# Optimization experiments

Measured on AMD Instinct MI355X. Metric: run time of the kernel, lower is better.

## Reference

```python
import jax, jax.numpy as jnp
import numpy as np

E, C_IN, NUM_CLASSES = 4, 3, 100
HW = 32
C1, C2, GC = 64, 128, 16
FC_IN = C2 * (HW // 4) * (HW // 4)  # 128*8*8 = 8192


def _conv(x, w, b):
    # x: [B,Cin,H,W], w: [Cout,Cin,3,3] -> [B,Cout,H,W] (SAME padding)
    y = jax.lax.conv_general_dilated(x, w, (1, 1), 'SAME',
                                     dimension_numbers=('NCHW', 'OIHW', 'NCHW'))
    return y + b[None, :, None, None]


def _maxpool2(x):
    return jax.lax.reduce_window(x, -jnp.inf, jax.lax.max,
                                 (1, 1, 2, 2), (1, 1, 2, 2), 'VALID')


def setup_inputs() -> dict:
    key = jax.random.key(0)
    ks = jax.random.split(key, 12)
    s = lambda k, shape, fan: (jax.random.normal(k, shape, jnp.float32) / np.sqrt(fan))
    return {
        'x': jax.random.normal(ks[0], (1024, C_IN, HW, HW), jnp.float32),
        # gating network
        'gate_cw': s(ks[1], (GC, C_IN, 3, 3), C_IN * 9),
        'gate_cb': jnp.zeros((GC,), jnp.float32),
        'gate_fw': s(ks[2], (E, GC), GC),
        'gate_fb': jnp.zeros((E,), jnp.float32),
        # stacked expert params [E, ...]
        'e_c1w': s(ks[3], (E, C1, C_IN, 3, 3), C_IN * 9),
        'e_c1b': jnp.zeros((E, C1), jnp.float32),
        'e_c2w': s(ks[4], (E, C2, C1, 3, 3), C1 * 9),
        'e_c2b': jnp.zeros((E, C2), jnp.float32),
        'e_fw': s(ks[5], (E, NUM_CLASSES, FC_IN), FC_IN),
        'e_fb': jnp.zeros((E, NUM_CLASSES), jnp.float32),
    }


def reference(x, gate_cw, gate_cb, gate_fw, gate_fb,
              e_c1w, e_c1b, e_c2w, e_c2b, e_fw, e_fb):
    B = x.shape[0]
    # --- gating: conv -> relu -> global avg pool -> linear -> softmax ---
    g = jax.nn.relu(_conv(x, gate_cw, gate_cb))            # [B,GC,H,W]
    g = g.mean(axis=(2, 3))                                # [B,GC]
    router_probs = jax.nn.softmax(g @ gate_fw.T + gate_fb) # [B,E]

    best_weights = router_probs.max(axis=1)                # [B]
    best_indices = jnp.argmax(router_probs, axis=1)        # [B]

    # --- hard top-1 dispatch: mask-and-combine (same math as gather/scatter) ---
    final_output = jnp.zeros((B, NUM_CLASSES), x.dtype)
    for e in range(E):  # fixed small expert count, structurally distinct params
        h = jax.nn.relu(_conv(x, e_c1w[e], e_c1b[e]))      # [B,64,32,32]
        h = _maxpool2(h)                                   # [B,64,16,16]
        h = jax.nn.relu(_conv(h, e_c2w[e], e_c2b[e]))      # [B,128,16,16]
        h = _maxpool2(h)                                   # [B,128,8,8]
        logits = h.reshape(B, -1) @ e_fw[e].T + e_fb[e]    # [B,100]
        mask = (best_indices == e)[:, None]
        final_output = final_output + jnp.where(
            mask, logits * best_weights[:, None], 0.0)

    mean_probs = router_probs.mean(axis=0)
    aux_loss = jnp.mean((mean_probs - 1.0 / E) ** 2)
    return final_output, router_probs, aux_loss
```

## Files before the change

### kernel.cpp

```cpp
#include <hip/hip_runtime.h>
#include <hip/hip_bf16.h>
#include <cstdint>


#define B_TOT 1024

typedef __attribute__((ext_vector_type(8))) short short8;
typedef __attribute__((ext_vector_type(16))) float f32x16;

__device__ __forceinline__ ushort f2bf(float f) {
  uint32_t u = __float_as_uint(f);
  u += 0x7fffu + ((u >> 16) & 1u);
  return (ushort)(u >> 16);
}

__global__ __launch_bounds__(256) void k_prep(
    const float* __restrict__ x, const float* __restrict__ gcw,
    const float* __restrict__ gcb, const float* __restrict__ gfw,
    const float* __restrict__ gfb, float* __restrict__ probs,
    float* __restrict__ best_w, int* __restrict__ best_idx,
    const float* __restrict__ w2, ushort* __restrict__ wp,
    const float* __restrict__ w1, ushort* __restrict__ wA,
    const float* __restrict__ efw, ushort* __restrict__ wfc) {
  __shared__ float xs[3 * 34 * 34];
  __shared__ float red[4 * 16];
  __shared__ float gm[16];
  __shared__ float lgs[4];
  const int blk = blockIdx.x;
  const int t = threadIdx.x;

  if (blk < 1024) {
    const int b = blk;
    const float* xb = x + (size_t)b * 3072;

    for (int c = t; c < 3468; c += 256) {
      const int ci = c / 1156;
      const int rem = c - ci * 1156;
      const int y = rem / 34;
      const int xx = rem - y * 34;
      const int gy = y - 1, gx = xx - 1;
      float v = 0.f;
      if (gy >= 0 && gy < 32 && gx >= 0 && gx < 32) v = xb[ci * 1024 + gy * 32 + gx];
      xs[c] = v;
    }
    __syncthreads();

    const int r = t >> 3;
    const int c0 = (t & 7) * 4;

    float accp[16][4];
#pragma unroll
    for (int c = 0; c < 16; c++)
#pragma unroll
      for (int p = 0; p < 4; p++) accp[c][p] = 0.f;

#pragma unroll
    for (int ci = 0; ci < 3; ci++) {
      float pv[3][6];
#pragma unroll
      for (int dy = 0; dy < 3; dy++) {
        const float* row = xs + ci * 1156 + (r + dy) * 34 + c0;
#pragma unroll
        for (int dx = 0; dx < 6; dx++) pv[dy][dx] = row[dx];
      }
#pragma unroll
      for (int c = 0; c < 16; c++) {
        const float* wr = gcw + (c * 3 + ci) * 9;
#pragma unroll
        for (int ky = 0; ky < 3; ky++)
#pragma unroll
          for (int kx = 0; kx < 3; kx++) {
            const float wv = wr[ky * 3 + kx];
#pragma unroll
            for (int p = 0; p < 4; p++)
              accp[c][p] += wv * pv[ky][kx + p];
          }
      }
    }

    float sums[16];
#pragma unroll
    for (int c = 0; c < 16; c++) {
      const float bb = gcb[c];
      float s = 0.f;
#pragma unroll
      for (int p = 0; p < 4; p++) s += fmaxf(accp[c][p] + bb, 0.f);
      sums[c] = s;
    }

    const int wave = t >> 6, lane = t & 63;
#pragma unroll
    for (int c = 0; c < 16; c++) {
      float v = sums[c];
      for (int o = 32; o > 0; o >>= 1) v += __shfl_down(v, o);
      if (lane == 0) red[wave * 16 + c] = v;
    }
    __syncthreads();
    if (t < 16)
      gm[t] = (red[t] + red[16 + t] + red[32 + t] + red[48 + t]) * (1.f / 1024.f);
    __syncthreads();
    if (t < 4) {
      float sum = gfb[t];
#pragma unroll
      for (int c = 0; c < 16; c++) sum += gm[c] * gfw[t * 16 + c];
      lgs[t] = sum;
    }
    __syncthreads();
    if (t == 0) {
      const float m = fmaxf(fmaxf(lgs[0], lgs[1]), fmaxf(lgs[2], lgs[3]));
      float ex[4], ssum = 0.f;
#pragma unroll
      for (int e = 0; e < 4; e++) { ex[e] = __expf(lgs[e] - m); ssum += ex[e]; }
      const float inv = 1.f / ssum;
      int bi = 0; float bp = ex[0];
#pragma unroll
      for (int e = 1; e < 4; e++) if (ex[e] > bp) { bp = ex[e]; bi = e; }
#pragma unroll
      for (int e = 0; e < 4; e++) probs[b * 4 + e] = ex[e] * inv;
      best_w[b] = bp * inv;
      best_idx[b] = bi;
    }
  } else if (blk < 2176) {
    const int i = (blk - 1024) * 256 + t;
    const int j = i & 7;
    const int cout = (i >> 3) & 127;
    const int kb = (i >> 10) & 7;
    const int kkE = i >> 13;
    const int kk = kkE - (kkE / 9) * 9;
    const int e = kkE / 9;
    const int ci = kb * 8 + j;
    const float f = w2[(size_t)(((e * 128 + cout) * 64 + ci) * 9) + kk];
    wp[i] = f2bf(f);
  } else if (blk < 2304) {
    const int i = (blk - 2176) * 256 + t;
    const int j = i & 7;
    const int cout = (i >> 3) & 63;
    const int kb = (i >> 9) & 3;
    const int e = i >> 11;
    const int k = kb * 8 + j;
    float f = 0.f;
    if (k < 27) {
      const int ci = k / 9;
      const int kk = k - ci * 9;
      f = w1[(size_t)(((e * 64 + cout) * 3 + ci) * 9) + kk];
    }
    wA[i] = f2bf(f);
  } else {
    const int i = (blk - 2304) * 256 + t;
    const int j = i & 7;
    const int cout = (i >> 3) & 127;
    const int kb = (i >> 10) & 1023;
    const int e = i >> 20;
    const int k = kb * 8 + j;
    float f = 0.f;
    if (cout < 100) f = efw[((size_t)(e * 100 + cout)) * 8192 + k];
    wfc[i] = f2bf(f);
  }
}

__global__ __launch_bounds__(256) void k_route(
    const float* __restrict__ probs, const int* __restrict__ best_idx_g,
    int* __restrict__ off_g, int* __restrict__ counts_g,
    int* __restrict__ order, float* __restrict__ aux_out) {
  __shared__ int cnt[4], ofs[5], cl[4];
  __shared__ short bidx[1024];
  __shared__ float red[16];
  const int t = threadIdx.x;
  if (t < 4) { cnt[t] = 0; cl[t] = 0; }
  __syncthreads();

  float asum[4] = {0.f, 0.f, 0.f, 0.f};
  for (int s = t; s < B_TOT; s += 256) {
    const int bi = best_idx_g[s];
    bidx[s] = (short)bi;
    atomicAdd(&cnt[bi], 1);
#pragma unroll
    for (int e = 0; e < 4; e++) asum[e] += probs[s * 4 + e];
  }
  __syncthreads();

  if (t == 0) {
    int o = 0;
#pragma unroll
    for (int e = 0; e < 4; e++) { ofs[e] = o; o += ((cnt[e] + 31) & ~31); }
    ofs[4] = o;
#pragma unroll
    for (int i = 0; i < 5; i++) off_g[i] = ofs[i];
#pragma unroll
    for (int e = 0; e < 4; e++) counts_g[e] = cnt[e];
  }
  __syncthreads();

  for (int s = t; s < B_TOT; s += 256) {
    const int e2 = bidx[s];
    const int slot = ofs[e2] + atomicAdd(&cl[e2], 1);
    order[slot] = s;
  }

  const int wave = t >> 6, lane = t & 63;
#pragma unroll
  for (int e = 0; e < 4; e++) {
    float v = asum[e];
    for (int o = 32; o > 0; o >>= 1) v += __shfl_down(v, o);
    if (lane == 0) red[wave * 4 + e] = v;
  }
  __syncthreads();
  if (t == 0) {
    float aux = 0.f;
#pragma unroll
    for (int e = 0; e < 4; e++) {
      const float mp = (red[e] + red[4 + e] + red[8 + e] + red[12 + e]) * (1.f / 1024.f);
      const float d = mp - 0.25f;
      aux += d * d;
    }
    aux_out[0] = aux * 0.25f;
  }
}

__global__ __launch_bounds__(256) void k_conv1(
    const float* __restrict__ x, const ushort* __restrict__ wA,
    const float* __restrict__ b1, const int* __restrict__ best_idx,
    ushort* __restrict__ h1q) {
  __shared__ ushort xs[3 * 34 * 34];
  __shared__ __align__(16) ushort Bl[256 * 32];
  const int b = blockIdx.x;
  const int t = threadIdx.x;
  const int e = __builtin_amdgcn_readfirstlane(best_idx[b]);
  const float* xb = x + (size_t)b * 3072;
  const float* b1e = b1 + (size_t)e * 64;

  for (int c = t; c < 3468; c += 256) {
    const int ci = c / 1156;
    const int rem = c - ci * 1156;
    const int y = rem / 34;
    const int xx = rem - y * 34;
    const int gy = y - 1, gx = xx - 1;
    float v = 0.f;
    if (gy >= 0 && gy < 32 && gx >= 0 && gx < 32) v = xb[ci * 1024 + gy * 32 + gx];
    xs[c] = f2bf(v);
  }

  const int lane = t & 63;
  const int wv = t >> 6;
  const int g = wv & 1;
  const int nh = wv >> 1;
  const int ln = lane & 31;
  const int half = lane >> 5;
  const int rr = t >> 5, cc = t & 31;

  const short8 af0 = *(const short8*)(wA + (size_t)(((e * 4 + half) * 64) + g * 32 + ln) * 8);
  const short8 af1 = *(const short8*)(wA + (size_t)(((e * 4 + 2 + half) * 64) + g * 32 + ln) * 8);

  float bias[16];
#pragma unroll
  for (int r = 0; r < 16; r++)
    bias[r] = b1e[g * 32 + (r & 3) + 8 * (r >> 2) + 4 * half];

#pragma unroll 1
  for (int s = 0; s < 4; s++) {
    __syncthreads();
    {
      ushort us[32];
#pragma unroll
      for (int k = 0; k < 32; k++) {
        ushort v = 0;
        if (k < 27) {
          const int ci = k / 9;
          const int tap = k - ci * 9;
          const int dy = tap / 3, dx = tap - dy * 3;
          v = xs[ci * 1156 + (8 * s + rr + dy) * 34 + cc + dx];
        }
        us[k] = v;
      }
      uint4 pk[2];
      uint* pu = (uint*)pk;
#pragma unroll
      for (int w = 0; w < 8; w++)
        pu[w] = (uint)us[w * 2] | ((uint)us[w * 2 + 1] << 16);
      *(uint4*)(Bl + t * 32) = pk[0];
      *(uint4*)(Bl + t * 32 + 8) = pk[1];
      uint4 pk2[2];
      uint* pu2 = (uint*)pk2;
#pragma unroll
      for (int w = 0; w < 8; w++)
        pu2[w] = (uint)us[16 + w * 2] | ((uint)us[16 + w * 2 + 1] << 16);
      *(uint4*)(Bl + t * 32 + 16) = pk2[0];
      *(uint4*)(Bl + t * 32 + 24) = pk2[1];
    }
    __syncthreads();

    f32x16 acc[4];
#pragma unroll
    for (int tt = 0; tt < 4; tt++)
#pragma unroll
      for (int i = 0; i < 16; i++) acc[tt][i] = 0.f;

#pragma unroll
    for (int tt = 0; tt < 4; tt++) {
      const ushort* bcol = Bl + (size_t)((nh * 4 + tt) * 32 + ln) * 32;
      const short8 b0 = *(const short8*)(bcol + half * 8);
      const short8 b1v = *(const short8*)(bcol + 16 + half * 8);
      acc[tt] = __builtin_amdgcn_mfma_f32_32x32x16_bf16(af0, b0, acc[tt], 0, 0, 0);
      acc[tt] = __builtin_amdgcn_mfma_f32_32x32x16_bf16(af1, b1v, acc[tt], 0, 0, 0);
    }

    const int pc = ln >> 1;
#pragma unroll
    for (int j = 0; j < 2; j++) {
      float pw[16];
#pragma unroll
      for (int r = 0; r < 16; r++) {
        float v = fmaxf(acc[2 * j][r], acc[2 * j + 1][r]);
        v = fmaxf(v, __shfl_xor(v, 1));
        pw[r] = fmaxf(v + bias[r], 0.f);
      }
      if ((lane & 1) == 0) {
        const int pos = (4 * s + nh * 2 + j) * 16 + pc;
        ushort* dst = h1q + (size_t)b * 16384 + pos * 8 + 4 * half;
#pragma unroll
        for (int rg = 0; rg < 4; rg++) {
          uint2 pk;
          pk.x = (uint)f2bf(pw[rg * 4 + 0]) | ((uint)f2bf(pw[rg * 4 + 1]) << 16);
          pk.y = (uint)f2bf(pw[rg * 4 + 2]) | ((uint)f2bf(pw[rg * 4 + 3]) << 16);
          *(uint2*)(dst + (g * 4 + rg) * 2048) = pk;
        }
      }
    }
  }
}

__global__ __launch_bounds__(512, 2) void k_conv2(
    const ushort* __restrict__ h1q, const ushort* __restrict__ wp,
    const float* __restrict__ b2, const int* __restrict__ best_idx,
    ushort* __restrict__ h2q) {
  __shared__ uint4 st[1440];
  const int blk = blockIdx.x;
  const int b = blk >> 1;
  const int q = blk & 1;
  const int t = threadIdx.x;
  const int e = __builtin_amdgcn_readfirstlane(best_idx[b]);
  const ushort* wpe = wp + (size_t)e * 73728;

  for (int c = t; c < 1440; c += 512) {
    const int row = c / 144;
    const int rem = c - row * 144;
    const int cig = rem / 18;
    const int col = rem - cig * 18;
    const int gy = 8 * q - 1 + row, gx = col - 1;
    uint4 v = make_uint4(0u, 0u, 0u, 0u);
    if (gy >= 0 && gy < 16 && gx >= 0 && gx < 16)
      v = *(const uint4*)(h1q + (size_t)b * 16384 + cig * 2048 + (gy * 16 + gx) * 8);
    st[c] = v;
  }
  __syncthreads();

  const int lane = t & 63;
  const int wv = t >> 6;
  const int g = wv & 1;
  const int h = wv >> 1;
  const int half = lane >> 5;
  const int n = lane & 31;
  const int drow = n >> 4;
  const int col15 = n & 15;
  const int cm0 = g * 64;

  const short* sbs = (const short*)st;
  const ushort* abase = wpe + (size_t)(half * 128 + cm0 + n) * 8;

  f32x16 acc[2];
#pragma unroll
  for (int m = 0; m < 2; m++)
#pragma unroll
    for (int i = 0; i < 16; i++) acc[m][i] = 0.f;

  short8 a0[4], a1[4];
#pragma unroll
  for (int c4 = 0; c4 < 4; c4++) {
    a0[c4] = *(const short8*)(abase + c4 * 2048);
    a1[c4] = *(const short8*)(abase + c4 * 2048 + 256);
  }

#pragma unroll
  for (int kk = 0; kk < 9; kk++) {
    const int ky = kk / 3;
    const int kx = kk - ky * 3;
#pragma unroll
    for (int c4 = 0; c4 < 4; c4++) {
      const int kb = c4 * 2 + half;
      const int rin = 2 * h + drow + ky;
      const int cin = col15 + kx;
      const short8 bf = *(const short8*)(sbs + ((rin * 8 + kb) * 18 + cin) * 8);
      acc[0] = __builtin_amdgcn_mfma_f32_32x32x16_bf16(a0[c4], bf, acc[0], 0, 0, 0);
      acc[1] = __builtin_amdgcn_mfma_f32_32x32x16_bf16(a1[c4], bf, acc[1], 0, 0, 0);
      if (kk < 8) {
        a0[c4] = *(const short8*)(abase + (kk + 1) * 8192 + c4 * 2048);
        a1[c4] = *(const short8*)(abase + (kk + 1) * 8192 + c4 * 2048 + 256);
      }
    }
  }
  __syncthreads();

  ushort* pls = (ushort*)st;
#pragma unroll
  for (int m = 0; m < 2; m++) {
#pragma unroll
    for (int r = 0; r < 16; r++) {
      float v = acc[m][r];
      v = fmaxf(v, __shfl_xor(v, 1));
      v = fmaxf(v, __shfl_xor(v, 16));
      if ((lane & 17) == 0) {
        const int rowm = (r & 3) + 8 * (r >> 2) + 4 * half;
        const int cout = cm0 + m * 32 + rowm;
        const int prl = h;
        const int pc = (n >> 1) & 7;
        pls[cout * 32 + prl * 8 + pc] = f2bf(fmaxf(v + b2[e * 128 + cout], 0.f));
      }
    }
  }
  __syncthreads();

  {
    const int f16 = t;
    const int flat = f16 * 8;
    const int cout = flat >> 5;
    const int pos32 = flat & 31;
    uint4* dst = (uint4*)(h2q + (size_t)b * 8192 + cout * 64 + 32 * q + pos32);
    *dst = ((const uint4*)pls)[f16];
  }
}

__global__ __launch_bounds__(256) void k_fc(
    const ushort* __restrict__ h2q, const ushort* __restrict__ wfc,
    const int* __restrict__ order, const int* __restrict__ off,
    const int* __restrict__ counts, float* __restrict__ partial) {
  __shared__ ushort bs[32 * 32 * 8];
  __shared__ int sid[32];
  const int tix = blockIdx.x;
  const int ks = blockIdx.y;
  const int base = tix * 32;
  if (base >= off[4]) return;
  int e = 0;
#pragma unroll
  for (int i = 1; i < 4; i++) if (base >= off[i]) e = i;
  const int vend = off[e] + counts[e];
  const int t = threadIdx.x;
  if (t < 32) {
    const int pos = base + t;
    sid[t] = (pos < vend) ? order[pos] : -1;
  }
  __syncthreads();

  const int lane = t & 63;
  const int wv = t >> 6;
  const int half = lane >> 5;
  const int mn = lane & 31;
  const int cout0 = wv * 32;
  const int ss = t & 31;
  const int kgrp = t >> 5;
  const int srow = sid[ss] >= 0 ? sid[ss] : 0;
  const ushort* arow = h2q + (size_t)srow * 8192;

  f32x16 acc;
#pragma unroll
  for (int i = 0; i < 16; i++) acc[i] = 0.f;

  const ushort* wbase = wfc + ((size_t)e * 1024 + (size_t)ks * 64) * 1024;
  const short* sb = (const short*)bs;

#pragma unroll
  for (int ch = 0; ch < 2; ch++) {
    const int k0g = ks * 512 + ch * 256;
    if (ch) __syncthreads();
#pragma unroll
    for (int p = 0; p < 4; p++) {
      const int kb = p * 8 + kgrp;
      const uint4 v = *(const uint4*)(arow + k0g + kb * 8);
      *(uint4*)(bs + (kb * 32 + ss) * 8) = v;
    }
    __syncthreads();
#pragma unroll
    for (int kk = 0; kk < 16; kk++) {
      const int kbl = kk * 2 + half;
      const short8 af = *(const short8*)(wbase +
          ((size_t)(ch * 32 + kbl) * 128 + cout0 + mn) * 8);
      const short8 bf = *(const short8*)(sb + (kbl * 32 + mn) * 8);
      acc = __builtin_amdgcn_mfma_f32_32x32x16_bf16(af, bf, acc, 0, 0, 0);
    }
  }

  float* pks = partial + (size_t)ks * 147456;
#pragma unroll
  for (int r = 0; r < 16; r++) {
    const int cout = cout0 + (r & 3) + 8 * (r >> 2) + 4 * half;
    pks[(size_t)cout * 1152 + base + mn] = acc[r];
  }
}

__global__ __launch_bounds__(256) void k_red(
    const float* __restrict__ partial, const float* __restrict__ efb,
    const int* __restrict__ order, const int* __restrict__ off,
    const int* __restrict__ counts, const float* __restrict__ best_w,
    float* __restrict__ out) {
  const int slot = blockIdx.x * 256 + threadIdx.x;
  if (slot >= off[4]) return;
  int e = 0;
#pragma unroll
  for (int i = 1; i < 4; i++) if (slot >= off[i]) e = i;
  if (slot - off[e] >= counts[e]) return;
  const int s = order[slot];
  const float bw = best_w[s];
  const int o0 = blockIdx.y * 4;
#pragma unroll
  for (int j = 0; j < 4; j++) {
    const int o = o0 + j;
    float sum = 0.f;
#pragma unroll
    for (int ks = 0; ks < 16; ks++)
      sum += partial[(size_t)ks * 147456 + (size_t)o * 1152 + slot];
    out[(size_t)s * 100 + o] = (sum + efb[e * 100 + o]) * bw;
  }
}

extern "C" void kernel_launch(void* const* d_in, const int* in_sizes, int n_in,
                              void* d_out, int out_size, void* d_ws, size_t ws_size,
                              hipStream_t stream) {
  const float* x   = (const float*)d_in[0];
  const float* gcw = (const float*)d_in[1];
  const float* gcb = (const float*)d_in[2];
  const float* gfw = (const float*)d_in[3];
  const float* gfb = (const float*)d_in[4];
  const float* c1w = (const float*)d_in[5];
  const float* c1b = (const float*)d_in[6];
  const float* c2w = (const float*)d_in[7];
  const float* c2b = (const float*)d_in[8];
  const float* efw = (const float*)d_in[9];
  const float* efb = (const float*)d_in[10];
  float* out = (float*)d_out;
  float* ws  = (float*)d_ws;

  float*  best_w   = ws + 16384;
  int*    best_idx = (int*)(ws + 17408);
  int*    counts   = (int*)(ws + 18432);
  int*    off      = (int*)(ws + 18440);
  int*    order    = (int*)(ws + 18448);
  ushort* wp       = (ushort*)(ws + 20480);
  ushort* wfc      = (ushort*)(ws + 167936);
  ushort* h1       = (ushort*)(ws + 2265088);
  ushort* h2q      = (ushort*)(ws + 10653696);
  float*  partial  = ws + 14848000;
  ushort* wA       = (ushort*)(ws + 17207296);

  float* probs = out + 102400;
  float* aux   = out + 106496;

  k_prep<<<18688, 256, 0, stream>>>(x, gcw, gcb, gfw, gfb, probs, best_w,
                                    best_idx, c2w, wp, c1w, wA, efw, wfc);
  k_route<<<1, 256, 0, stream>>>(probs, best_idx, off, counts, order, aux);
  k_conv1<<<1024, 256, 0, stream>>>(x, wA, c1b, best_idx, h1);
  k_conv2<<<2048, 512, 0, stream>>>(h1, wp, c2b, best_idx, h2q);
  dim3 g5(36, 16);
  k_fc<<<g5, 256, 0, stream>>>(h2q, wfc, order, off, counts, partial);
  dim3 g6(5, 25);
  k_red<<<g6, 256, 0, stream>>>(partial, efb, order, off, counts, best_w, out);
}
```

Baseline: 216.7 us.

## Split conv1 into four row-strip blocks and remap conv2 waves to share A fragments

conv1 now launches four blocks per image, each staging only a 10-row haloed strip and doing a single im2col+MFMA pass instead of looping over four strips serially. This gives more parallelism and less shared memory per block, at the cost of redundant halo loads and repeated weight-fragment loads. In conv2 each wave now owns one 32-channel output tile and two spatial tiles, so each loaded A fragment is reused across two B reads instead of the reverse. That halves the per-wave weight register footprint and global weight loads, but doubles the LDS B-fragment reads.

```diff
diff --git a/kernel.cpp b/kernel.cpp
--- a/kernel.cpp
+++ b/kernel.cpp
@@ -221,24 +221,58 @@
     const float* __restrict__ x, const ushort* __restrict__ wA,
     const float* __restrict__ b1, const int* __restrict__ best_idx,
     ushort* __restrict__ h1q) {
-  __shared__ ushort xs[3 * 34 * 34];
+  __shared__ ushort xs[1020];
   __shared__ __align__(16) ushort Bl[256 * 32];
-  const int b = blockIdx.x;
+  const int blk = blockIdx.x;
+  const int b = blk >> 2;
+  const int q = blk & 3;
   const int t = threadIdx.x;
   const int e = __builtin_amdgcn_readfirstlane(best_idx[b]);
   const float* xb = x + (size_t)b * 3072;
   const float* b1e = b1 + (size_t)e * 64;
 
-  for (int c = t; c < 3468; c += 256) {
-    const int ci = c / 1156;
-    const int rem = c - ci * 1156;
-    const int y = rem / 34;
-    const int xx = rem - y * 34;
-    const int gy = y - 1, gx = xx - 1;
+  for (int c = t; c < 1020; c += 256) {
+    const int ci = c / 340;
+    const int rem = c - ci * 340;
+    const int hr = rem / 34;
+    const int hc = rem - hr * 34;
+    const int gr = 8 * q + hr - 1, gc = hc - 1;
     float v = 0.f;
-    if (gy >= 0 && gy < 32 && gx >= 0 && gx < 32) v = xb[ci * 1024 + gy * 32 + gx];
+    if (gr >= 0 && gr < 32 && gc >= 0 && gc < 32) v = xb[ci * 1024 + gr * 32 + gc];
     xs[c] = f2bf(v);
   }
+  __syncthreads();
+
+  {
+    const int rr = t >> 5, cc = t & 31;
+    ushort us[32];
+#pragma unroll
+    for (int k = 0; k < 32; k++) {
+      ushort v = 0;
+      if (k < 27) {
+        const int ci = k / 9;
+        const int tap = k - ci * 9;
+        const int dy = tap / 3, dx = tap - dy * 3;
+        v = xs[ci * 340 + (rr + dy) * 34 + cc + dx];
+      }
+      us[k] = v;
+    }
+    uint4 pk[2];
+    uint* pu = (uint*)pk;
+#pragma unroll
+    for (int w = 0; w < 8; w++)
+      pu[w] = (uint)us[w * 2] | ((uint)us[w * 2 + 1] << 16);
+    *(uint4*)(Bl + t * 32) = pk[0];
+    *(uint4*)(Bl + t * 32 + 8) = pk[1];
+    uint4 pk2[2];
+    uint* pu2 = (uint*)pk2;
+#pragma unroll
+    for (int w = 0; w < 8; w++)
+      pu2[w] = (uint)us[16 + w * 2] | ((uint)us[16 + w * 2 + 1] << 16);
+    *(uint4*)(Bl + t * 32 + 16) = pk2[0];
+    *(uint4*)(Bl + t * 32 + 24) = pk2[1];
+  }
+  __syncthreads();
 
   const int lane = t & 63;
   const int wv = t >> 6;
@@ -246,84 +280,49 @@
   const int nh = wv >> 1;
   const int ln = lane & 31;
   const int half = lane >> 5;
-  const int rr = t >> 5, cc = t & 31;
 
   const short8 af0 = *(const short8*)(wA + (size_t)(((e * 4 + half) * 64) + g * 32 + ln) * 8);
   const short8 af1 = *(const short8*)(wA + (size_t)(((e * 4 + 2 + half) * 64) + g * 32 + ln) * 8);
 
+  f32x16 acc[4];
+#pragma unroll
+  for (int tt = 0; tt < 4; tt++)
+#pragma unroll
+    for (int i = 0; i < 16; i++) acc[tt][i] = 0.f;
+
+#pragma unroll
+  for (int tt = 0; tt < 4; tt++) {
+    const ushort* bcol = Bl + (size_t)((nh * 4 + tt) * 32 + ln) * 32;
+    const short8 b0 = *(const short8*)(bcol + half * 8);
+    const short8 b1v = *(const short8*)(bcol + 16 + half * 8);
+    acc[tt] = __builtin_amdgcn_mfma_f32_32x32x16_bf16(af0, b0, acc[tt], 0, 0, 0);
+    acc[tt] = __builtin_amdgcn_mfma_f32_32x32x16_bf16(af1, b1v, acc[tt], 0, 0, 0);
+  }
+
   float bias[16];
 #pragma unroll
   for (int r = 0; r < 16; r++)
     bias[r] = b1e[g * 32 + (r & 3) + 8 * (r >> 2) + 4 * half];
 
-#pragma unroll 1
-  for (int s = 0; s < 4; s++) {
-    __syncthreads();
-    {
-      ushort us[32];
-#pragma unroll
-      for (int k = 0; k < 32; k++) {
-        ushort v = 0;
-        if (k < 27) {
-          const int ci = k / 9;
-          const int tap = k - ci * 9;
-          const int dy = tap / 3, dx = tap - dy * 3;
-          v = xs[ci * 1156 + (8 * s + rr + dy) * 34 + cc + dx];
-        }
-        us[k] = v;
-      }
-      uint4 pk[2];
-      uint* pu = (uint*)pk;
-#pragma unroll
-      for (int w = 0; w < 8; w++)
-        pu[w] = (uint)us[w * 2] | ((uint)us[w * 2 + 1] << 16);
-      *(uint4*)(Bl + t * 32) = pk[0];
-      *(uint4*)(Bl + t * 32 + 8) = pk[1];
-      uint4 pk2[2];
-      uint* pu2 = (uint*)pk2;
-#pragma unroll
-      for (int w = 0; w < 8; w++)
-        pu2[w] = (uint)us[16 + w * 2] | ((uint)us[16 + w * 2 + 1] << 16);
-      *(uint4*)(Bl + t * 32 + 16) = pk2[0];
-      *(uint4*)(Bl + t * 32 + 24) = pk2[1];
-    }
-    __syncthreads();
-
-    f32x16 acc[4];
-#pragma unroll
-    for (int tt = 0; tt < 4; tt++)
-#pragma unroll
-      for (int i = 0; i < 16; i++) acc[tt][i] = 0.f;
-
-#pragma unroll
-    for (int tt = 0; tt < 4; tt++) {
-      const ushort* bcol = Bl + (size_t)((nh * 4 + tt) * 32 + ln) * 32;
-      const short8 b0 = *(const short8*)(bcol + half * 8);
-      const short8 b1v = *(const short8*)(bcol + 16 + half * 8);
-      acc[tt] = __builtin_amdgcn_mfma_f32_32x32x16_bf16(af0, b0, acc[tt], 0, 0, 0);
-      acc[tt] = __builtin_amdgcn_mfma_f32_32x32x16_bf16(af1, b1v, acc[tt], 0, 0, 0);
-    }
-
-    const int pc = ln >> 1;
-#pragma unroll
-    for (int j = 0; j < 2; j++) {
-      float pw[16];
-#pragma unroll
-      for (int r = 0; r < 16; r++) {
-        float v = fmaxf(acc[2 * j][r], acc[2 * j + 1][r]);
-        v = fmaxf(v, __shfl_xor(v, 1));
-        pw[r] = fmaxf(v + bias[r], 0.f);
-      }
-      if ((lane & 1) == 0) {
-        const int pos = (4 * s + nh * 2 + j) * 16 + pc;
-        ushort* dst = h1q + (size_t)b * 16384 + pos * 8 + 4 * half;
-#pragma unroll
-        for (int rg = 0; rg < 4; rg++) {
-          uint2 pk;
-          pk.x = (uint)f2bf(pw[rg * 4 + 0]) | ((uint)f2bf(pw[rg * 4 + 1]) << 16);
-          pk.y = (uint)f2bf(pw[rg * 4 + 2]) | ((uint)f2bf(pw[rg * 4 + 3]) << 16);
-          *(uint2*)(dst + (g * 4 + rg) * 2048) = pk;
-        }
+  const int pc = ln >> 1;
+#pragma unroll
+  for (int j = 0; j < 2; j++) {
+    float pw[16];
+#pragma unroll
+    for (int r = 0; r < 16; r++) {
+      float v = fmaxf(acc[2 * j][r], acc[2 * j + 1][r]);
+      v = fmaxf(v, __shfl_xor(v, 1));
+      pw[r] = fmaxf(v + bias[r], 0.f);
+    }
+    if ((lane & 1) == 0) {
+      const int pos = (4 * q + nh * 2 + j) * 16 + pc;
+      ushort* dst = h1q + (size_t)b * 16384 + pos * 8 + 4 * half;
+#pragma unroll
+      for (int rg = 0; rg < 4; rg++) {
+        uint2 pk;
+        pk.x = (uint)f2bf(pw[rg * 4 + 0]) | ((uint)f2bf(pw[rg * 4 + 1]) << 16);
+        pk.y = (uint)f2bf(pw[rg * 4 + 2]) | ((uint)f2bf(pw[rg * 4 + 3]) << 16);
+        *(uint2*)(dst + (g * 4 + rg) * 2048) = pk;
       }
     }
   }
@@ -356,29 +355,26 @@
 
   const int lane = t & 63;
   const int wv = t >> 6;
-  const int g = wv & 1;
-  const int h = wv >> 1;
+  const int m = wv & 3;
+  const int h2 = wv >> 2;
   const int half = lane >> 5;
   const int n = lane & 31;
   const int drow = n >> 4;
   const int col15 = n & 15;
-  const int cm0 = g * 64;
 
   const short* sbs = (const short*)st;
-  const ushort* abase = wpe + (size_t)(half * 128 + cm0 + n) * 8;
+  const ushort* abase = wpe + (size_t)(half * 128 + m * 32 + n) * 8;
 
   f32x16 acc[2];
 #pragma unroll
-  for (int m = 0; m < 2; m++)
-#pragma unroll
-    for (int i = 0; i < 16; i++) acc[m][i] = 0.f;
-
-  short8 a0[4], a1[4];
-#pragma unroll
-  for (int c4 = 0; c4 < 4; c4++) {
-    a0[c4] = *(const short8*)(abase + c4 * 2048);
-    a1[c4] = *(const short8*)(abase + c4 * 2048 + 256);
-  }
+  for (int nt = 0; nt < 2; nt++)
+#pragma unroll
+    for (int i = 0; i < 16; i++) acc[nt][i] = 0.f;
+
+  short8 a[4];
+#pragma unroll
+  for (int c4 = 0; c4 < 4; c4++)
+    a[c4] = *(const short8*)(abase + c4 * 2048);
 
 #pragma unroll
   for (int kk = 0; kk < 9; kk++) {
@@ -387,14 +383,15 @@
 #pragma unroll
     for (int c4 = 0; c4 < 4; c4++) {
       const int kb = c4 * 2 + half;
-      const int rin = 2 * h + drow + ky;
-      const int cin = col15 + kx;
-      const short8 bf = *(const short8*)(sbs + ((rin * 8 + kb) * 18 + cin) * 8);
-      acc[0] = __builtin_amdgcn_mfma_f32_32x32x16_bf16(a0[c4], bf, acc[0], 0, 0, 0);
-      acc[1] = __builtin_amdgcn_mfma_f32_32x32x16_bf16(a1[c4], bf, acc[1], 0, 0, 0);
+#pragma unroll
+      for (int nt = 0; nt < 2; nt++) {
+        const int rin = 4 * h2 + 2 * nt + drow + ky;
+        const int cin = col15 + kx;
+        const short8 bf = *(const short8*)(sbs + ((rin * 8 + kb) * 18 + cin) * 8);
+        acc[nt] = __builtin_amdgcn_mfma_f32_32x32x16_bf16(a[c4], bf, acc[nt], 0, 0, 0);
+      }
       if (kk < 8) {
-        a0[c4] = *(const short8*)(abase + (kk + 1) * 8192 + c4 * 2048);
-        a1[c4] = *(const short8*)(abase + (kk + 1) * 8192 + c4 * 2048 + 256);
+        a[c4] = *(const short8*)(abase + (kk + 1) * 8192 + c4 * 2048);
       }
     }
   }
@@ -402,16 +399,16 @@
 
   ushort* pls = (ushort*)st;
 #pragma unroll
-  for (int m = 0; m < 2; m++) {
+  for (int nt = 0; nt < 2; nt++) {
 #pragma unroll
     for (int r = 0; r < 16; r++) {
-      float v = acc[m][r];
+      float v = acc[nt][r];
       v = fmaxf(v, __shfl_xor(v, 1));
       v = fmaxf(v, __shfl_xor(v, 16));
       if ((lane & 17) == 0) {
         const int rowm = (r & 3) + 8 * (r >> 2) + 4 * half;
-        const int cout = cm0 + m * 32 + rowm;
-        const int prl = h;
+        const int cout = m * 32 + rowm;
+        const int prl = 2 * h2 + nt;
         const int pc = (n >> 1) & 7;
         pls[cout * 32 + prl * 8 + pc] = f2bf(fmaxf(v + b2[e * 128 + cout], 0.f));
       }
@@ -556,7 +553,7 @@
   k_prep<<<18688, 256, 0, stream>>>(x, gcw, gcb, gfw, gfb, probs, best_w,
                                     best_idx, c2w, wp, c1w, wA, efw, wfc);
   k_route<<<1, 256, 0, stream>>>(probs, best_idx, off, counts, order, aux);
-  k_conv1<<<1024, 256, 0, stream>>>(x, wA, c1b, best_idx, h1);
+  k_conv1<<<4096, 256, 0, stream>>>(x, wA, c1b, best_idx, h1);
   k_conv2<<<2048, 512, 0, stream>>>(h1, wp, c2b, best_idx, h2q);
   dim3 g5(36, 16);
   k_fc<<<g5, 256, 0, stream>>>(h2q, wfc, order, off, counts, partial);
```

Measured after the change: 214.4 us. No clear change (-1.0%).
